# Optimization experiments

Hardware: AMD Instinct MI355X
Metric: run time of the kernel (lower is better)

## Reference

```python
import jax, jax.numpy as jnp
import numpy as np

B, M, F = 32, 32768, 256


def setup_inputs() -> dict:
    key = jax.random.key(0)
    ks = jax.random.split(key, 6)
    scale1 = 1.0 / np.sqrt(2 * F)
    scale2 = 1.0 / np.sqrt(F)
    return {
        "input_data": jax.random.normal(ks[0], (B, F), dtype=jnp.float32),
        "memory": jax.random.normal(ks[1], (M, F), dtype=jnp.float32),
        "W1": jax.random.uniform(ks[2], (F, 2 * F), jnp.float32, -scale1, scale1),
        "b1": jax.random.uniform(ks[3], (F,), jnp.float32, -scale1, scale1),
        "W2": jax.random.uniform(ks[4], (1, F), jnp.float32, -scale2, scale2),
        "b2": jax.random.uniform(ks[5], (1,), jnp.float32, -scale2, scale2),
        # threshold below 1/M so the conditional scatter-write path actually fires
        # (torch default 0.05 with random weights never writes for M=32768)
        "threshold": jnp.float32(1e-5),
    }


def reference(input_data, memory, W1, b1, W2, b2, threshold):
    # Linear on cat([x, mem]) splits into two independent matmuls.
    W1x, W1m = W1[:, :F], W1[:, F:]          # each [F, F]
    hx = input_data @ W1x.T                   # [B, F]
    hm = memory @ W1m.T                       # [M, F]
    h = jnp.tanh(hx[:, None, :] + hm[None, :, :] + b1)  # [B, M, F]
    scores = h @ W2[0] + b2[0]                # [B, M]
    weights = jax.nn.softmax(scores, axis=1)  # softmax over memory slots
    best = jnp.argmax(weights, axis=1)        # [B] winning slot per item
    maxw = jnp.max(weights, axis=1)           # [B]
    mask = maxw > threshold                   # write only if above threshold
    # Sequential loop semantics: later batch items overwrite earlier ones
    # at the same slot. last[s] = 1 + index of last masked writer to slot s.
    order = jnp.where(mask, jnp.arange(B, dtype=jnp.int32) + 1, 0)
    last = jax.ops.segment_max(order, best, num_segments=M)  # [M]
    last = jnp.maximum(last, 0)
    src = input_data[jnp.maximum(last - 1, 0)]               # [M, F]
    updated_memory = jnp.where((last > 0)[:, None], src, memory)
    return updated_memory
```

## Files before the change

### kernel.cpp

```cpp
#include <hip/hip_runtime.h>

#define FDIM 256
#define BDIM 32
#define MDIM 32768
#define NB   512

#define WS_EM    0
#define WS_EX    (WS_EM + MDIM*FDIM)
#define WS_W2N   (WS_EX + BDIM*FDIM)
#define WS_PMAX  (WS_W2N + FDIM)
#define WS_PSUM  (WS_PMAX + BDIM*NB)
#define WS_PARG  (WS_PSUM + BDIM*NB)
#define WS_WIN   (WS_PARG + BDIM*NB)
#define WS_BEST  (WS_WIN + 32)
#define WS_GMAX  (WS_BEST + 32)
#define WS_GSUM  (WS_GMAX + 32)
#define WS_GARG  (WS_GSUM + 32)
#define WS_WH    (WS_GARG + 32)
#define WS_WL    (WS_WH + 32768)

#define C2 2.8853900817779268f

typedef __attribute__((ext_vector_type(8))) short bf16x8;
typedef __attribute__((ext_vector_type(8))) unsigned short ushort8;
typedef __attribute__((ext_vector_type(4))) float f32x4;

__device__ inline unsigned short f2bf(float x) {
  unsigned u = __float_as_uint(x);
  return (unsigned short)((u + 0x7fffu + ((u >> 16) & 1u)) >> 16);
}
__device__ inline float bf2f(unsigned short h) {
  return __uint_as_float(((unsigned)h) << 16);
}

__global__ __launch_bounds__(256) void k1_prep(const float* __restrict__ input,
                                               const float* __restrict__ W1,
                                               const float* __restrict__ b1,
                                               const float* __restrict__ W2,
                                               float* __restrict__ Ex,
                                               float* __restrict__ w2n,
                                               unsigned short* __restrict__ wh,
                                               unsigned short* __restrict__ wl) {
  if (blockIdx.x < BDIM) {
    const int b = blockIdx.x, f = threadIdx.x;
    const float* in = input + b * FDIM;
    const float* w  = W1 + (size_t)f * 512;
    float acc = b1[f];
    #pragma unroll 8
    for (int k = 0; k < FDIM; k += 4) {
      float4 iv = *(const float4*)(in + k);
      float4 wv = *(const float4*)(w + k);
      acc = fmaf(iv.x, wv.x, acc); acc = fmaf(iv.y, wv.y, acc);
      acc = fmaf(iv.z, wv.z, acc); acc = fmaf(iv.w, wv.w, acc);
    }
    Ex[b * FDIM + f] = __builtin_amdgcn_exp2f(acc * C2);
    if (b == 0) w2n[f] = -2.0f * W2[f];
  } else {
    int id = ((blockIdx.x - BDIM) * 256 + threadIdx.x) * 4;
    int f = id >> 8, c = id & 255;
    float4 v = *(const float4*)(W1 + (size_t)f * 512 + 256 + c);
    float xs[4] = {v.x, v.y, v.z, v.w};
    #pragma unroll
    for (int e = 0; e < 4; ++e) {
      unsigned short h = f2bf(xs[e]);
      wh[id + e] = h;
      wl[id + e] = f2bf(xs[e] - bf2f(h));
    }
  }
}

__global__ __launch_bounds__(512, 4) void k23_fused(const float* __restrict__ mem,
                                                    const unsigned short* __restrict__ wh,
                                                    const unsigned short* __restrict__ wl,
                                                    const float* __restrict__ Ex,
                                                    const float* __restrict__ w2n,
                                                    float* __restrict__ pmax,
                                                    float* __restrict__ psum,
                                                    int* __restrict__ parg,
                                                    float* __restrict__ out) {
  __shared__ __align__(16) char smem[69632];
  unsigned short* AH = (unsigned short*)(smem);
  unsigned short* AL = (unsigned short*)(smem + 5120);
  unsigned short* BH = (unsigned short*)(smem + 10240);
  unsigned short* BL = (unsigned short*)(smem + 30720);
  float* emT = (float*)smem;

  const int tid = threadIdx.x;
  const int lane = tid & 63, wid = tid >> 6;
  const int m0 = blockIdx.x * 64;
  const int rb = lane & 15, g8 = (lane >> 4) * 8;
  const int mh = wid & 1;
  const int fq = wid >> 1;

  f32x4 acc[2][4];
  #pragma unroll
  for (int i = 0; i < 2; ++i)
    #pragma unroll
    for (int j = 0; j < 4; ++j) acc[i][j] = (f32x4){0.f, 0.f, 0.f, 0.f};

  for (int s = 0; s < 8; ++s) {
    const int k0 = s * 32;
    __syncthreads();
    if (tid < 256) {
      int r = tid >> 2, c8 = (tid & 3) * 8;
      const float* mrow = mem + (size_t)(m0 + r) * 256 + k0 + c8;
      float4 a0 = *(const float4*)(mrow);
      float4 a1 = *(const float4*)(mrow + 4);
      float* orow = out + (size_t)(m0 + r) * 256 + k0 + c8;
      *(float4*)(orow)     = a0;
      *(float4*)(orow + 4) = a1;
      float xs[8] = {a0.x, a0.y, a0.z, a0.w, a1.x, a1.y, a1.z, a1.w};
      ushort8 ahv, alv;
      #pragma unroll
      for (int e = 0; e < 8; ++e) {
        unsigned short h = f2bf(xs[e]);
        ahv[e] = h;
        alv[e] = f2bf(xs[e] - bf2f(h));
      }
      *(ushort8*)&AH[r * 40 + c8] = ahv;
      *(ushort8*)&AL[r * 40 + c8] = alv;
    } else {
      int t2 = tid - 256;
      #pragma unroll
      for (int q = 0; q < 4; ++q) {
        int id = q * 256 + t2, br = id >> 2, bc = (id & 3) * 8;
        *(uint4*)&BH[br * 40 + bc] = *(const uint4*)(wh + (size_t)br * 256 + k0 + bc);
        *(uint4*)&BL[br * 40 + bc] = *(const uint4*)(wl + (size_t)br * 256 + k0 + bc);
      }
    }
    __syncthreads();

    bf16x8 fah[2], fal[2], fbh[4], fbl[4];
    #pragma unroll
    for (int i = 0; i < 2; ++i) {
      fah[i] = *(const bf16x8*)&AH[(mh * 32 + i * 16 + rb) * 40 + g8];
      fal[i] = *(const bf16x8*)&AL[(mh * 32 + i * 16 + rb) * 40 + g8];
    }
    #pragma unroll
    for (int j = 0; j < 4; ++j) {
      fbh[j] = *(const bf16x8*)&BH[(fq * 64 + j * 16 + rb) * 40 + g8];
      fbl[j] = *(const bf16x8*)&BL[(fq * 64 + j * 16 + rb) * 40 + g8];
    }
    #pragma unroll
    for (int i = 0; i < 2; ++i)
      #pragma unroll
      for (int j = 0; j < 4; ++j) {
        acc[i][j] = __builtin_amdgcn_mfma_f32_16x16x32_bf16(fah[i], fbh[j], acc[i][j], 0, 0, 0);
        acc[i][j] = __builtin_amdgcn_mfma_f32_16x16x32_bf16(fah[i], fbl[j], acc[i][j], 0, 0, 0);
        acc[i][j] = __builtin_amdgcn_mfma_f32_16x16x32_bf16(fal[i], fbh[j], acc[i][j], 0, 0, 0);
      }
  }

  __syncthreads();
  #pragma unroll
  for (int j = 0; j < 4; ++j)
    #pragma unroll
    for (int i = 0; i < 2; ++i) {
      const int fl = fq * 64 + j * 16 + rb;
      const int mloc = mh * 32 + i * 16 + (lane >> 4) * 4;
      float4 v;
      v.x = __builtin_amdgcn_exp2f(acc[i][j][0] * C2);
      v.y = __builtin_amdgcn_exp2f(acc[i][j][1] * C2);
      v.z = __builtin_amdgcn_exp2f(acc[i][j][2] * C2);
      v.w = __builtin_amdgcn_exp2f(acc[i][j][3] * C2);
      *(float4*)(emT + fl * 68 + mloc) = v;
    }
  __syncthreads();

  const int wuid = __builtin_amdgcn_readfirstlane(wid);
  const float* ex0 = Ex + (size_t)(wuid * 4 + 0) * FDIM;
  const float* ex1 = Ex + (size_t)(wuid * 4 + 1) * FDIM;
  const float* ex2 = Ex + (size_t)(wuid * 4 + 2) * FDIM;
  const float* ex3 = Ex + (size_t)(wuid * 4 + 3) * FDIM;

  float acc0 = 0.f, acc1 = 0.f, acc2 = 0.f, acc3 = 0.f;
  #pragma unroll 2
  for (int f = 0; f < FDIM; f += 4) {
    float e0 = emT[(f + 0) * 68 + lane];
    float e1 = emT[(f + 1) * 68 + lane];
    float e2 = emT[(f + 2) * 68 + lane];
    float e3 = emT[(f + 3) * 68 + lane];
    float w0 = w2n[f + 0], w1 = w2n[f + 1];
    float w2 = w2n[f + 2], w3 = w2n[f + 3];
    #define SCORE4(exP, accV)                                            \
    {                                                                    \
      float u0 = fmaf(e0, exP[f + 0], 1.f);                              \
      float u1 = fmaf(e1, exP[f + 1], 1.f);                              \
      float u2 = fmaf(e2, exP[f + 2], 1.f);                              \
      float u3 = fmaf(e3, exP[f + 3], 1.f);                              \
      float p01 = u0 * u1, p23 = u2 * u3;                                \
      float den = p01 * p23;                                             \
      float t0 = fmaf(w1, u0, w0 * u1);                                  \
      float t1 = fmaf(w3, u2, w2 * u3);                                  \
      float num = fmaf(t1, p01, t0 * p23);                               \
      accV = fmaf(num, __builtin_amdgcn_rcpf(den), accV);                \
    }
    SCORE4(ex0, acc0)
    SCORE4(ex1, acc1)
    SCORE4(ex2, acc2)
    SCORE4(ex3, acc3)
    #undef SCORE4
  }

  float accb[4] = {acc0, acc1, acc2, acc3};
  const int blk = blockIdx.x;
  #pragma unroll
  for (int bi = 0; bi < 4; ++bi) {
    float s = accb[bi]; int idx = m0 + lane;
    #pragma unroll
    for (int off = 32; off > 0; off >>= 1) {
      float so = __shfl_xor(s, off);
      int   io = __shfl_xor(idx, off);
      if (so > s || (so == s && io < idx)) { s = so; idx = io; }
    }
    float ex = __expf(accb[bi] - s);
    #pragma unroll
    for (int off = 32; off > 0; off >>= 1) ex += __shfl_xor(ex, off);
    if (lane == 0) {
      int b = wuid * 4 + bi;
      pmax[b * NB + blk] = s;
      psum[b * NB + blk] = ex;
      parg[b * NB + blk] = idx;
    }
  }
}

__global__ __launch_bounds__(256) void k4a_reduce(const float* __restrict__ pmax,
                                                  const float* __restrict__ psum,
                                                  const int* __restrict__ parg,
                                                  float* __restrict__ gmax,
                                                  float* __restrict__ gsum,
                                                  int* __restrict__ garg) {
  __shared__ float sm[4], ss[4];
  __shared__ int   sa[4];
  const int b = blockIdx.x, tid = threadIdx.x;
  float cm = -3.0e38f, cs = 0.f; int ca = 0x7fffffff;
  #pragma unroll
  for (int t = 0; t < NB / 256; ++t) {
    int i = t * 256 + tid;
    float s = pmax[b * NB + i];
    float p = psum[b * NB + i];
    int   a = parg[b * NB + i];
    if (s > cm)      { cs = cs * __expf(cm - s) + p; cm = s; ca = a; }
    else if (s == cm){ cs += p; if (a < ca) ca = a; }
    else             { cs += p * __expf(s - cm); }
  }
  #pragma unroll
  for (int off = 32; off > 0; off >>= 1) {
    float om = __shfl_xor(cm, off);
    float os = __shfl_xor(cs, off);
    int   oa = __shfl_xor(ca, off);
    if (om > cm)      { cs = cs * __expf(cm - om) + os; cm = om; ca = oa; }
    else if (om == cm){ cs += os; if (oa < ca) ca = oa; }
    else              { cs += os * __expf(om - cm); }
  }
  if ((tid & 63) == 0) { sm[tid >> 6] = cm; ss[tid >> 6] = cs; sa[tid >> 6] = ca; }
  __syncthreads();
  if (tid == 0) {
    cm = sm[0]; cs = ss[0]; ca = sa[0];
    for (int w = 1; w < 4; ++w) {
      float om = sm[w], os = ss[w]; int oa = sa[w];
      if (om > cm)      { cs = cs * __expf(cm - om) + os; cm = om; ca = oa; }
      else if (om == cm){ cs += os; if (oa < ca) ca = oa; }
      else              { cs += os * __expf(om - cm); }
    }
    gmax[b] = cm; gsum[b] = cs; garg[b] = ca;
  }
}

__global__ __launch_bounds__(64) void k4b_select(const float* __restrict__ gsum,
                                                 const int* __restrict__ garg,
                                                 const float* __restrict__ thr_p,
                                                 int* __restrict__ win,
                                                 int* __restrict__ best) {
  const int tid = threadIdx.x;
  if (tid < BDIM) {
    const float thr = *thr_p;
    int me = garg[tid];
    int w = (1.0f / gsum[tid] > thr) ? 1 : 0;
    if (w) {
      for (int b2 = tid + 1; b2 < BDIM; ++b2)
        if ((1.0f / gsum[b2] > thr) && garg[b2] == me) { w = 0; break; }
    }
    win[tid] = w; best[tid] = me;
  }
}

__global__ __launch_bounds__(64) void k6_patch(const float* __restrict__ input,
                                               const int* __restrict__ win,
                                               const int* __restrict__ best,
                                               float* __restrict__ out) {
  const int b = blockIdx.x;
  if (!win[b]) return;
  const int m = best[b];
  const int t = threadIdx.x;
  *(float4*)(out + (size_t)m * 256 + t * 4) = *(const float4*)(input + (size_t)b * 256 + t * 4);
}

extern "C" void kernel_launch(void* const* d_in, const int* in_sizes, int n_in,
                              void* d_out, int out_size, void* d_ws, size_t ws_size,
                              hipStream_t stream) {
  const float* input  = (const float*)d_in[0];
  const float* memory = (const float*)d_in[1];
  const float* W1     = (const float*)d_in[2];
  const float* b1     = (const float*)d_in[3];
  const float* W2     = (const float*)d_in[4];
  const float* thr    = (const float*)d_in[6];

  float* ws   = (float*)d_ws;
  float* Ex   = ws + WS_EX;
  float* w2n  = ws + WS_W2N;
  float* pmax = ws + WS_PMAX;
  float* psum = ws + WS_PSUM;
  int*   parg = (int*)(ws + WS_PARG);
  int*   win  = (int*)(ws + WS_WIN);
  int*   best = (int*)(ws + WS_BEST);
  float* gmax = ws + WS_GMAX;
  float* gsum = ws + WS_GSUM;
  int*   garg = (int*)(ws + WS_GARG);
  unsigned short* wh = (unsigned short*)(ws + WS_WH);
  unsigned short* wl = (unsigned short*)(ws + WS_WL);
  float* out  = (float*)d_out;

  hipLaunchKernelGGL(k1_prep,    dim3(BDIM + 64), dim3(256), 0, stream, input, W1, b1, W2, Ex, w2n, wh, wl);
  hipLaunchKernelGGL(k23_fused,  dim3(MDIM / 64), dim3(512), 0, stream, memory, wh, wl, Ex, w2n, pmax, psum, parg, out);
  hipLaunchKernelGGL(k4a_reduce, dim3(BDIM),      dim3(256), 0, stream, pmax, psum, parg, gmax, gsum, garg);
  hipLaunchKernelGGL(k4b_select, dim3(1),         dim3(64),  0, stream, gsum, garg, thr, win, best);
  hipLaunchKernelGGL(k6_patch,   dim3(BDIM),      dim3(64),  0, stream, input, win, best, out);
}
```

Before: 71.71 us.

## Prefetch next K-slice into registers and fuse select with patch kernel

The fused projection/score kernel now issues the global loads for the next K-slice of memory and weights into registers before running the MFMA work on the current slice. The registers are then written to shared memory after the next barrier, so global latency overlaps with compute. It also merges the winner-selection kernel and the patch kernel into one launch, with each block deciding its own write, which removes one launch and the win/best workspace round trip. The cost is more register pressure from the staging buffers in a 512-thread block, plus an extra barrier per iteration.

```diff
diff --git a/kernel.cpp b/kernel.cpp
--- a/kernel.cpp
+++ b/kernel.cpp
@@ -92,24 +92,34 @@
   const int mh = wid & 1;
   const int fq = wid >> 1;
 
-  f32x4 acc[2][4];
-  #pragma unroll
-  for (int i = 0; i < 2; ++i)
-    #pragma unroll
-    for (int j = 0; j < 4; ++j) acc[i][j] = (f32x4){0.f, 0.f, 0.f, 0.f};
-
-  for (int s = 0; s < 8; ++s) {
+  float4 pa0, pa1;
+  uint4  pb[8];
+  const int ar = tid >> 2, ac8 = (tid & 3) * 8;
+  const int bt2 = tid - 256;
+
+  auto LOADS = [&](int s) {
     const int k0 = s * 32;
-    __syncthreads();
     if (tid < 256) {
-      int r = tid >> 2, c8 = (tid & 3) * 8;
-      const float* mrow = mem + (size_t)(m0 + r) * 256 + k0 + c8;
-      float4 a0 = *(const float4*)(mrow);
-      float4 a1 = *(const float4*)(mrow + 4);
-      float* orow = out + (size_t)(m0 + r) * 256 + k0 + c8;
-      *(float4*)(orow)     = a0;
-      *(float4*)(orow + 4) = a1;
-      float xs[8] = {a0.x, a0.y, a0.z, a0.w, a1.x, a1.y, a1.z, a1.w};
+      const float* mrow = mem + (size_t)(m0 + ar) * 256 + k0 + ac8;
+      pa0 = *(const float4*)(mrow);
+      pa1 = *(const float4*)(mrow + 4);
+    } else {
+      #pragma unroll
+      for (int q = 0; q < 4; ++q) {
+        int id = q * 256 + bt2, br = id >> 2, bc = (id & 3) * 8;
+        pb[q * 2 + 0] = *(const uint4*)(wh + (size_t)br * 256 + k0 + bc);
+        pb[q * 2 + 1] = *(const uint4*)(wl + (size_t)br * 256 + k0 + bc);
+      }
+    }
+  };
+
+  auto WRITES = [&](int s) {
+    const int k0 = s * 32;
+    if (tid < 256) {
+      float* orow = out + (size_t)(m0 + ar) * 256 + k0 + ac8;
+      *(float4*)(orow)     = pa0;
+      *(float4*)(orow + 4) = pa1;
+      float xs[8] = {pa0.x, pa0.y, pa0.z, pa0.w, pa1.x, pa1.y, pa1.z, pa1.w};
       ushort8 ahv, alv;
       #pragma unroll
       for (int e = 0; e < 8; ++e) {
@@ -117,18 +127,30 @@
         ahv[e] = h;
         alv[e] = f2bf(xs[e] - bf2f(h));
       }
-      *(ushort8*)&AH[r * 40 + c8] = ahv;
-      *(ushort8*)&AL[r * 40 + c8] = alv;
+      *(ushort8*)&AH[ar * 40 + ac8] = ahv;
+      *(ushort8*)&AL[ar * 40 + ac8] = alv;
     } else {
-      int t2 = tid - 256;
       #pragma unroll
       for (int q = 0; q < 4; ++q) {
-        int id = q * 256 + t2, br = id >> 2, bc = (id & 3) * 8;
-        *(uint4*)&BH[br * 40 + bc] = *(const uint4*)(wh + (size_t)br * 256 + k0 + bc);
-        *(uint4*)&BL[br * 40 + bc] = *(const uint4*)(wl + (size_t)br * 256 + k0 + bc);
+        int id = q * 256 + bt2, br = id >> 2, bc = (id & 3) * 8;
+        *(uint4*)&BH[br * 40 + bc] = pb[q * 2 + 0];
+        *(uint4*)&BL[br * 40 + bc] = pb[q * 2 + 1];
       }
     }
+  };
+
+  f32x4 acc[2][4];
+  #pragma unroll
+  for (int i = 0; i < 2; ++i)
+    #pragma unroll
+    for (int j = 0; j < 4; ++j) acc[i][j] = (f32x4){0.f, 0.f, 0.f, 0.f};
+
+  LOADS(0);
+  for (int s = 0; s < 8; ++s) {
     __syncthreads();
+    WRITES(s);
+    __syncthreads();
+    if (s < 7) LOADS(s + 1);
 
     bf16x8 fah[2], fal[2], fbh[4], fbl[4];
     #pragma unroll
@@ -268,33 +290,22 @@
   }
 }
 
-__global__ __launch_bounds__(64) void k4b_select(const float* __restrict__ gsum,
-                                                 const int* __restrict__ garg,
-                                                 const float* __restrict__ thr_p,
-                                                 int* __restrict__ win,
-                                                 int* __restrict__ best) {
-  const int tid = threadIdx.x;
-  if (tid < BDIM) {
-    const float thr = *thr_p;
-    int me = garg[tid];
-    int w = (1.0f / gsum[tid] > thr) ? 1 : 0;
-    if (w) {
-      for (int b2 = tid + 1; b2 < BDIM; ++b2)
-        if ((1.0f / gsum[b2] > thr) && garg[b2] == me) { w = 0; break; }
-    }
-    win[tid] = w; best[tid] = me;
-  }
-}
-
-__global__ __launch_bounds__(64) void k6_patch(const float* __restrict__ input,
-                                               const int* __restrict__ win,
-                                               const int* __restrict__ best,
-                                               float* __restrict__ out) {
+__global__ __launch_bounds__(64) void k5_select_patch(const float* __restrict__ gsum,
+                                                      const int* __restrict__ garg,
+                                                      const float* __restrict__ thr_p,
+                                                      const float* __restrict__ input,
+                                                      float* __restrict__ out) {
   const int b = blockIdx.x;
-  if (!win[b]) return;
-  const int m = best[b];
+  const float thr = *thr_p;
+  const int me = garg[b];
+  int w = (1.0f / gsum[b] > thr) ? 1 : 0;
+  if (w) {
+    for (int b2 = b + 1; b2 < BDIM; ++b2)
+      if ((1.0f / gsum[b2] > thr) && garg[b2] == me) { w = 0; break; }
+  }
+  if (!w) return;
   const int t = threadIdx.x;
-  *(float4*)(out + (size_t)m * 256 + t * 4) = *(const float4*)(input + (size_t)b * 256 + t * 4);
+  *(float4*)(out + (size_t)me * 256 + t * 4) = *(const float4*)(input + (size_t)b * 256 + t * 4);
 }
 
 extern "C" void kernel_launch(void* const* d_in, const int* in_sizes, int n_in,
@@ -313,8 +324,6 @@
   float* pmax = ws + WS_PMAX;
   float* psum = ws + WS_PSUM;
   int*   parg = (int*)(ws + WS_PARG);
-  int*   win  = (int*)(ws + WS_WIN);
-  int*   best = (int*)(ws + WS_BEST);
   float* gmax = ws + WS_GMAX;
   float* gsum = ws + WS_GSUM;
   int*   garg = (int*)(ws + WS_GARG);
@@ -325,6 +334,5 @@
   hipLaunchKernelGGL(k1_prep,    dim3(BDIM + 64), dim3(256), 0, stream, input, W1, b1, W2, Ex, w2n, wh, wl);
   hipLaunchKernelGGL(k23_fused,  dim3(MDIM / 64), dim3(512), 0, stream, memory, wh, wl, Ex, w2n, pmax, psum, parg, out);
   hipLaunchKernelGGL(k4a_reduce, dim3(BDIM),      dim3(256), 0, stream, pmax, psum, parg, gmax, gsum, garg);
-  hipLaunchKernelGGL(k4b_select, dim3(1),         dim3(64),  0, stream, gsum, garg, thr, win, best);
-  hipLaunchKernelGGL(k6_patch,   dim3(BDIM),      dim3(64),  0, stream, input, win, best, out);
-}
+  hipLaunchKernelGGL(k5_select_patch, dim3(BDIM), dim3(64),  0, stream, gsum, garg, thr, input, out);
+}
```

Measured after the change: 87.53 us. 22.1% more time.

## Halve emT LDS staging in two passes and fuse tail kernels into one

Applied to the files above, without the earlier changes.

The fused score kernel now stages the exp values into shared memory in two 128-feature halves instead of all 256 at once. This cuts LDS from 68 KB to 50 KB per block, which may allow more resident blocks per CU, at the cost of two extra barriers. Separately, the three small tail kernels (reduce, select, patch) are merged into one 1024-thread single-block kernel, removing two launches and their global-memory round trips.

```diff
diff --git a/kernel.cpp b/kernel.cpp
--- a/kernel.cpp
+++ b/kernel.cpp
@@ -78,7 +78,7 @@
                                                     float* __restrict__ psum,
                                                     int* __restrict__ parg,
                                                     float* __restrict__ out) {
-  __shared__ __align__(16) char smem[69632];
+  __shared__ __align__(16) char smem[51200];
   unsigned short* AH = (unsigned short*)(smem);
   unsigned short* AL = (unsigned short*)(smem + 5120);
   unsigned short* BH = (unsigned short*)(smem + 10240);
@@ -151,55 +151,61 @@
       }
   }
 
-  __syncthreads();
-  #pragma unroll
-  for (int j = 0; j < 4; ++j)
-    #pragma unroll
-    for (int i = 0; i < 2; ++i) {
-      const int fl = fq * 64 + j * 16 + rb;
-      const int mloc = mh * 32 + i * 16 + (lane >> 4) * 4;
-      float4 v;
-      v.x = __builtin_amdgcn_exp2f(acc[i][j][0] * C2);
-      v.y = __builtin_amdgcn_exp2f(acc[i][j][1] * C2);
-      v.z = __builtin_amdgcn_exp2f(acc[i][j][2] * C2);
-      v.w = __builtin_amdgcn_exp2f(acc[i][j][3] * C2);
-      *(float4*)(emT + fl * 68 + mloc) = v;
-    }
-  __syncthreads();
-
   const int wuid = __builtin_amdgcn_readfirstlane(wid);
   const float* ex0 = Ex + (size_t)(wuid * 4 + 0) * FDIM;
   const float* ex1 = Ex + (size_t)(wuid * 4 + 1) * FDIM;
   const float* ex2 = Ex + (size_t)(wuid * 4 + 2) * FDIM;
   const float* ex3 = Ex + (size_t)(wuid * 4 + 3) * FDIM;
-
   float acc0 = 0.f, acc1 = 0.f, acc2 = 0.f, acc3 = 0.f;
-  #pragma unroll 2
-  for (int f = 0; f < FDIM; f += 4) {
-    float e0 = emT[(f + 0) * 68 + lane];
-    float e1 = emT[(f + 1) * 68 + lane];
-    float e2 = emT[(f + 2) * 68 + lane];
-    float e3 = emT[(f + 3) * 68 + lane];
-    float w0 = w2n[f + 0], w1 = w2n[f + 1];
-    float w2 = w2n[f + 2], w3 = w2n[f + 3];
-    #define SCORE4(exP, accV)                                            \
-    {                                                                    \
-      float u0 = fmaf(e0, exP[f + 0], 1.f);                              \
-      float u1 = fmaf(e1, exP[f + 1], 1.f);                              \
-      float u2 = fmaf(e2, exP[f + 2], 1.f);                              \
-      float u3 = fmaf(e3, exP[f + 3], 1.f);                              \
-      float p01 = u0 * u1, p23 = u2 * u3;                                \
-      float den = p01 * p23;                                             \
-      float t0 = fmaf(w1, u0, w0 * u1);                                  \
-      float t1 = fmaf(w3, u2, w2 * u3);                                  \
-      float num = fmaf(t1, p01, t0 * p23);                               \
-      accV = fmaf(num, __builtin_amdgcn_rcpf(den), accV);                \
-    }
-    SCORE4(ex0, acc0)
-    SCORE4(ex1, acc1)
-    SCORE4(ex2, acc2)
-    SCORE4(ex3, acc3)
-    #undef SCORE4
+
+  #pragma unroll
+  for (int h = 0; h < 2; ++h) {
+    __syncthreads();
+    if ((wid >> 2) == h) {
+      #pragma unroll
+      for (int j = 0; j < 4; ++j)
+        #pragma unroll
+        for (int i = 0; i < 2; ++i) {
+          const int fl = (fq * 64 + j * 16 + rb) - h * 128;
+          const int mloc = mh * 32 + i * 16 + (lane >> 4) * 4;
+          float4 v;
+          v.x = __builtin_amdgcn_exp2f(acc[i][j][0] * C2);
+          v.y = __builtin_amdgcn_exp2f(acc[i][j][1] * C2);
+          v.z = __builtin_amdgcn_exp2f(acc[i][j][2] * C2);
+          v.w = __builtin_amdgcn_exp2f(acc[i][j][3] * C2);
+          *(float4*)(emT + fl * 68 + mloc) = v;
+        }
+    }
+    __syncthreads();
+
+    #pragma unroll 2
+    for (int fl2 = 0; fl2 < 128; fl2 += 4) {
+      const int fg = h * 128 + fl2;
+      float e0 = emT[(fl2 + 0) * 68 + lane];
+      float e1 = emT[(fl2 + 1) * 68 + lane];
+      float e2 = emT[(fl2 + 2) * 68 + lane];
+      float e3 = emT[(fl2 + 3) * 68 + lane];
+      float w0 = w2n[fg + 0], w1 = w2n[fg + 1];
+      float w2 = w2n[fg + 2], w3 = w2n[fg + 3];
+      #define SCORE4(exP, accV)                                          \
+      {                                                                  \
+        float u0 = fmaf(e0, exP[fg + 0], 1.f);                           \
+        float u1 = fmaf(e1, exP[fg + 1], 1.f);                           \
+        float u2 = fmaf(e2, exP[fg + 2], 1.f);                           \
+        float u3 = fmaf(e3, exP[fg + 3], 1.f);                           \
+        float p01 = u0 * u1, p23 = u2 * u3;                              \
+        float den = p01 * p23;                                           \
+        float t0 = fmaf(w1, u0, w0 * u1);                                \
+        float t1 = fmaf(w3, u2, w2 * u3);                                \
+        float num = fmaf(t1, p01, t0 * p23);                             \
+        accV = fmaf(num, __builtin_amdgcn_rcpf(den), accV);              \
+      }
+      SCORE4(ex0, acc0)
+      SCORE4(ex1, acc1)
+      SCORE4(ex2, acc2)
+      SCORE4(ex3, acc3)
+      #undef SCORE4
+    }
   }
 
   float accb[4] = {acc0, acc1, acc2, acc3};
@@ -225,76 +231,62 @@
   }
 }
 
-__global__ __launch_bounds__(256) void k4a_reduce(const float* __restrict__ pmax,
-                                                  const float* __restrict__ psum,
-                                                  const int* __restrict__ parg,
-                                                  float* __restrict__ gmax,
-                                                  float* __restrict__ gsum,
-                                                  int* __restrict__ garg) {
-  __shared__ float sm[4], ss[4];
-  __shared__ int   sa[4];
-  const int b = blockIdx.x, tid = threadIdx.x;
-  float cm = -3.0e38f, cs = 0.f; int ca = 0x7fffffff;
+__global__ __launch_bounds__(1024) void k45_finish(const float* __restrict__ pmax,
+                                                   const float* __restrict__ psum,
+                                                   const int* __restrict__ parg,
+                                                   const float* __restrict__ thr_p,
+                                                   const float* __restrict__ input,
+                                                   float* __restrict__ out) {
+  __shared__ float gm[BDIM], gs[BDIM];
+  __shared__ int   ga[BDIM], wn[BDIM];
+  const int tid = threadIdx.x, lane = tid & 63, w = tid >> 6;
   #pragma unroll
-  for (int t = 0; t < NB / 256; ++t) {
-    int i = t * 256 + tid;
-    float s = pmax[b * NB + i];
-    float p = psum[b * NB + i];
-    int   a = parg[b * NB + i];
-    if (s > cm)      { cs = cs * __expf(cm - s) + p; cm = s; ca = a; }
-    else if (s == cm){ cs += p; if (a < ca) ca = a; }
-    else             { cs += p * __expf(s - cm); }
-  }
-  #pragma unroll
-  for (int off = 32; off > 0; off >>= 1) {
-    float om = __shfl_xor(cm, off);
-    float os = __shfl_xor(cs, off);
-    int   oa = __shfl_xor(ca, off);
-    if (om > cm)      { cs = cs * __expf(cm - om) + os; cm = om; ca = oa; }
-    else if (om == cm){ cs += os; if (oa < ca) ca = oa; }
-    else              { cs += os * __expf(om - cm); }
-  }
-  if ((tid & 63) == 0) { sm[tid >> 6] = cm; ss[tid >> 6] = cs; sa[tid >> 6] = ca; }
-  __syncthreads();
-  if (tid == 0) {
-    cm = sm[0]; cs = ss[0]; ca = sa[0];
-    for (int w = 1; w < 4; ++w) {
-      float om = sm[w], os = ss[w]; int oa = sa[w];
+  for (int half = 0; half < 2; ++half) {
+    const int b = w * 2 + half;
+    float cm = -3.0e38f, cs = 0.f; int ca = 0x7fffffff;
+    #pragma unroll
+    for (int t = 0; t < NB / 64; ++t) {
+      int i = t * 64 + lane;
+      float s = pmax[b * NB + i];
+      float p = psum[b * NB + i];
+      int   a = parg[b * NB + i];
+      if (s > cm)      { cs = cs * __expf(cm - s) + p; cm = s; ca = a; }
+      else if (s == cm){ cs += p; if (a < ca) ca = a; }
+      else             { cs += p * __expf(s - cm); }
+    }
+    #pragma unroll
+    for (int off = 32; off > 0; off >>= 1) {
+      float om = __shfl_xor(cm, off);
+      float os = __shfl_xor(cs, off);
+      int   oa = __shfl_xor(ca, off);
       if (om > cm)      { cs = cs * __expf(cm - om) + os; cm = om; ca = oa; }
       else if (om == cm){ cs += os; if (oa < ca) ca = oa; }
       else              { cs += os * __expf(om - cm); }
     }
-    gmax[b] = cm; gsum[b] = cs; garg[b] = ca;
-  }
-}
-
-__global__ __launch_bounds__(64) void k4b_select(const float* __restrict__ gsum,
-                                                 const int* __restrict__ garg,
-                                                 const float* __restrict__ thr_p,
-                                                 int* __restrict__ win,
-                                                 int* __restrict__ best) {
-  const int tid = threadIdx.x;
+    if (lane == 0) { gm[b] = cm; gs[b] = cs; ga[b] = ca; }
+  }
+  __syncthreads();
   if (tid < BDIM) {
     const float thr = *thr_p;
-    int me = garg[tid];
-    int w = (1.0f / gsum[tid] > thr) ? 1 : 0;
-    if (w) {
+    const int me = ga[tid];
+    int w_ = (1.0f / gs[tid] > thr) ? 1 : 0;
+    if (w_) {
       for (int b2 = tid + 1; b2 < BDIM; ++b2)
-        if ((1.0f / gsum[b2] > thr) && garg[b2] == me) { w = 0; break; }
-    }
-    win[tid] = w; best[tid] = me;
-  }
-}
-
-__global__ __launch_bounds__(64) void k6_patch(const float* __restrict__ input,
-                                               const int* __restrict__ win,
-                                               const int* __restrict__ best,
-                                               float* __restrict__ out) {
-  const int b = blockIdx.x;
-  if (!win[b]) return;
-  const int m = best[b];
-  const int t = threadIdx.x;
-  *(float4*)(out + (size_t)m * 256 + t * 4) = *(const float4*)(input + (size_t)b * 256 + t * 4);
+        if ((1.0f / gs[b2] > thr) && ga[b2] == me) { w_ = 0; break; }
+    }
+    wn[tid] = w_;
+  }
+  __syncthreads();
+  {
+    const int b = tid >> 5, sub = tid & 31;
+    if (wn[b]) {
+      const int m = ga[b];
+      *(float4*)(out + (size_t)m * 256 + sub * 8) =
+          *(const float4*)(input + (size_t)b * 256 + sub * 8);
+      *(float4*)(out + (size_t)m * 256 + sub * 8 + 4) =
+          *(const float4*)(input + (size_t)b * 256 + sub * 8 + 4);
+    }
+  }
 }
 
 extern "C" void kernel_launch(void* const* d_in, const int* in_sizes, int n_in,
@@ -313,18 +305,11 @@
   float* pmax = ws + WS_PMAX;
   float* psum = ws + WS_PSUM;
   int*   parg = (int*)(ws + WS_PARG);
-  int*   win  = (int*)(ws + WS_WIN);
-  int*   best = (int*)(ws + WS_BEST);
-  float* gmax = ws + WS_GMAX;
-  float* gsum = ws + WS_GSUM;
-  int*   garg = (int*)(ws + WS_GARG);
   unsigned short* wh = (unsigned short*)(ws + WS_WH);
   unsigned short* wl = (unsigned short*)(ws + WS_WL);
   float* out  = (float*)d_out;
 
-  hipLaunchKernelGGL(k1_prep,    dim3(BDIM + 64), dim3(256), 0, stream, input, W1, b1, W2, Ex, w2n, wh, wl);
-  hipLaunchKernelGGL(k23_fused,  dim3(MDIM / 64), dim3(512), 0, stream, memory, wh, wl, Ex, w2n, pmax, psum, parg, out);
-  hipLaunchKernelGGL(k4a_reduce, dim3(BDIM),      dim3(256), 0, stream, pmax, psum, parg, gmax, gsum, garg);
-  hipLaunchKernelGGL(k4b_select, dim3(1),         dim3(64),  0, stream, gsum, garg, thr, win, best);
-  hipLaunchKernelGGL(k6_patch,   dim3(BDIM),      dim3(64),  0, stream, input, win, best, out);
-}
+  hipLaunchKernelGGL(k1_prep,    dim3(BDIM + 64), dim3(256),  0, stream, input, W1, b1, W2, Ex, w2n, wh, wl);
+  hipLaunchKernelGGL(k23_fused,  dim3(MDIM / 64), dim3(512),  0, stream, memory, wh, wl, Ex, w2n, pmax, psum, parg, out);
+  hipLaunchKernelGGL(k45_finish, dim3(1),         dim3(1024), 0, stream, pmax, psum, parg, thr, input, out);
+}
```

Result: slower. 74.15 us (+3.4%).
